# Optimization experiments

Hardware: AMD Instinct MI355X
Metric: run time of the kernel (lower is better)

## Reference

```python
import jax, jax.numpy as jnp
import numpy as np

KERNELS = ("gaussian", "laplacian", "gaussian", "laplacian")
N, M, D, N_PER = 384, 384, 64, 200


def setup_inputs():
    key = jax.random.key(0)
    kx, ky, kb, kp = jax.random.split(key, 4)
    X = jax.random.normal(kx, (N, D), dtype=jnp.float32)
    Y = jax.random.normal(ky, (M, D), dtype=jnp.float32)
    # positive bandwidths of realistic magnitude for d=64 gaussian/laplacian kernels
    bandwidths = jax.random.uniform(kb, (4,), dtype=jnp.float32) * 8.0 + 4.0
    # each row is a random permutation of n+m indices (torch.randperm equivalent)
    perms = jax.vmap(lambda k: jax.random.permutation(k, N + M))(
        jax.random.split(kp, N_PER)).astype(jnp.int32)
    return {"X": X, "Y": Y, "bandwidths": bandwidths, "perms": perms}


def _pairwise_dist(Z):
    # torch.cdist(Z, Z, p=2); eps keeps sqrt grad finite on the zero diagonal
    sq = jnp.sum(Z * Z, axis=1)
    d2 = jnp.maximum(sq[:, None] + sq[None, :] - 2.0 * (Z @ Z.T), 0.0)
    return jnp.sqrt(d2 + 1e-12)


def reference(X, Y, bandwidths, perms):
    n, m = X.shape[0], Y.shape[0]
    Z = jnp.concatenate([X, Y], axis=0)            # [n+m, d]
    dist = _pairwise_dist(Z)                        # [n+m, n+m]
    idx = jnp.arange(min(n, m))
    perm_X, perm_Y = perms[:, :n], perms[:, n:]    # [n_per, n], [n_per, m]
    U, U_b = [], []
    for i, kern in enumerate(KERNELS):
        b = bandwidths[i]
        if kern == "gaussian":
            K = jnp.exp(-(dist * dist) / (b * b))
        else:  # laplacian
            K = jnp.exp(-dist / b)
        # mmd_u's in-place K_XY[diag]=0 mutates the view of K, so zero first
        K = K.at[idx, n + idx].set(0.0)
        K_XX, K_YY, K_XY = K[:n, :n], K[n:, n:], K[:n, n:]
        mmd = ((K_XX.sum() - jnp.trace(K_XX)) / (n * (n - 1))
               + (K_YY.sum() - jnp.trace(K_YY)) / (m * (m - 1))
               - 2.0 * K_XY.sum() / (n * m))
        U.append(mmd)
        # fast_perm: gather permuted blocks, zero diagonals, reduce per permutation
        diagK = jnp.diagonal(K)
        sXX = K[perm_X[:, :, None], perm_X[:, None, :]].sum((1, 2)) - diagK[perm_X].sum(1)
        sYY = K[perm_Y[:, :, None], perm_Y[:, None, :]].sum((1, 2)) - diagK[perm_Y].sum(1)
        sXY = (K[perm_X[:, :, None], perm_Y[:, None, :]].sum((1, 2))
               - K[perm_X[:, idx], perm_Y[:, idx]].sum(1))
        U_b.append(sXX / (n * (n - 1)) + sYY / (m * (m - 1)) - 2.0 * sXY / (n * m))
    U = jnp.stack(U)[:, None]    # [n_b, 1]  == compute_U_stats U.unsqueeze(1)
    U_b = jnp.stack(U_b)         # [n_b, n_per]
    return jnp.concatenate([U, U_b], axis=1)  # [n_b, 1 + n_per]
```

## Files before the change

### kernel.cpp

```cpp
#include <hip/hip_runtime.h>

#define NTOT 768
#define NHALF 384
#define DDIM 64
#define NPER 200
#define PPAD 256
#define NKER 4
#define NMB 12
#define NKH 2
#define NB_GEMM 384
#define NPART (NMB * NKH)
#define NTILE 12
#define LDSROW 68

typedef __attribute__((ext_vector_type(8))) short short8;
typedef __attribute__((ext_vector_type(4))) float floatx4;

constexpr int K0SZ  = NTOT * NTOT;
constexpr int OF_KH = 0;
constexpr int KH_FLOATS = NKER * K0SZ / 2;
constexpr int OF_P   = OF_KH + KH_FLOATS;
constexpr int OF_C   = OF_P + NKER * NTILE * NTOT;
constexpr int OF_ROWM = OF_C + NKER * NHALF;
constexpr int OF_COLM = OF_ROWM + NKER * NTOT;
constexpr int OF_SCAL = OF_COLM + NKER * NTOT;
constexpr int OF_STT  = OF_SCAL + 16;
constexpr int STT_FLOATS = PPAD * NTOT / 2;
constexpr int OF_Q0P  = OF_STT + STT_FLOATS;

__device__ __forceinline__ unsigned short f2bf(float f) {
    unsigned int u = __float_as_uint(f);
    return (unsigned short)((u + 0x7FFFu + ((u >> 16) & 1u)) >> 16);
}
__device__ __forceinline__ float bf2f(unsigned short h) {
    return __uint_as_float(((unsigned int)h) << 16);
}

__global__ __launch_bounds__(256) void k_s1(const float* __restrict__ X,
                                            const float* __restrict__ Y,
                                            const float* __restrict__ bw,
                                            const int* __restrict__ perms,
                                            float* __restrict__ ws) {
    __shared__ float smem[128 * LDSROW + 128];
    float* zb  = smem;
    float* nrm = smem + 128 * LDSROW;
    int bid = blockIdx.x, tid = threadIdx.x;
    unsigned short* STT = (unsigned short*)(ws + OF_STT);
    unsigned short* KH  = (unsigned short*)(ws + OF_KH);

    if (bid < NPER) {
        if (tid < 192) {
            ((uint2*)(STT + bid * NTOT))[tid] = make_uint2(0u, 0u);
            if (bid < PPAD - NPER)
                ((uint2*)(STT + (NPER + bid) * NTOT))[tid] = make_uint2(0u, 0u);
        }
        __syncthreads();
        int v = perms[bid * NTOT + tid];
        STT[bid * NTOT + v] = 0x3F80;
        if (tid < NHALF - 256) {
            int v2 = perms[bid * NTOT + 256 + tid];
            STT[bid * NTOT + v2] = 0x3F80;
        }
        return;
    }

    int t  = bid - NPER;
    int at = t / NTILE, bt = t % NTILE;
    int a0 = at * 64, b0 = bt * 64;
    int ta = tid >> 4, tb = tid & 15;

    float ib2[NKER], ib1[NKER];
#pragma unroll
    for (int k = 0; k < NKER; ++k) { float b = bw[k]; ib2[k] = 1.f / (b * b); ib1[k] = 1.f / b; }

#pragma unroll
    for (int it = 0; it < 8; ++it) {
        int idx = it * 256 + tid;
        int j = idx >> 4, qf = idx & 15;
        int g = (j < 64) ? a0 + j : b0 + (j - 64);
        const float* zr = (g < NHALF) ? X + g * DDIM : Y + (g - NHALF) * DDIM;
        *(float4*)(zb + j * LDSROW + qf * 4) = *(const float4*)(zr + qf * 4);
    }
    __syncthreads();
    if (tid < 128) {
        float s = 0.f;
        const float* zr = zb + tid * LDSROW;
#pragma unroll
        for (int d = 0; d < DDIM; d += 4) {
            float4 zv = *(const float4*)(zr + d);
            s += zv.x * zv.x + zv.y * zv.y + zv.z * zv.z + zv.w * zv.w;
        }
        nrm[tid] = s;
    }
    __syncthreads();

    float acc[4][4];
#pragma unroll
    for (int r = 0; r < 4; ++r)
#pragma unroll
        for (int c = 0; c < 4; ++c) acc[r][c] = 0.f;
#pragma unroll
    for (int s = 0; s < 16; ++s) {
        float4 av[4], bv[4];
#pragma unroll
        for (int r = 0; r < 4; ++r) av[r] = *(const float4*)(zb + (ta * 4 + r) * LDSROW + s * 4);
#pragma unroll
        for (int c = 0; c < 4; ++c) bv[c] = *(const float4*)(zb + (64 + tb * 4 + c) * LDSROW + s * 4);
#pragma unroll
        for (int r = 0; r < 4; ++r)
#pragma unroll
            for (int c = 0; c < 4; ++c) {
                acc[r][c] = fmaf(av[r].x, bv[c].x, acc[r][c]);
                acc[r][c] = fmaf(av[r].y, bv[c].y, acc[r][c]);
                acc[r][c] = fmaf(av[r].z, bv[c].z, acc[r][c]);
                acc[r][c] = fmaf(av[r].w, bv[c].w, acc[r][c]);
            }
    }

    float rs[4][NKER];
#pragma unroll
    for (int r = 0; r < 4; ++r)
#pragma unroll
        for (int k = 0; k < NKER; ++k) rs[r][k] = 0.f;

#pragma unroll
    for (int r = 0; r < 4; ++r) {
        int a = a0 + ta * 4 + r;
        ushort4 us[NKER];
#pragma unroll
        for (int c = 0; c < 4; ++c) {
            int b = b0 + tb * 4 + c;
            float d2 = (nrm[ta * 4 + r] + nrm[64 + tb * 4 + c]) - 2.f * acc[r][c];
            if (b == a) d2 = 0.f;
            d2 = fmaxf(d2, 0.f);
            float d2e = d2 + 1e-12f;
            float dist = sqrtf(d2e);
#pragma unroll
            for (int k = 0; k < NKER; ++k) {
                float val = ((k & 1) == 0) ? __expf(-d2e * ib2[k]) : __expf(-dist * ib1[k]);
                rs[r][k] += val;
                unsigned short h = f2bf(val);
                if (c == 0) us[k].x = h; else if (c == 1) us[k].y = h;
                else if (c == 2) us[k].z = h; else us[k].w = h;
                if (bt == at + 6 && tb == ta && c == r)
                    ws[OF_C + k * NHALF + a] = val;
            }
        }
#pragma unroll
        for (int k = 0; k < NKER; ++k)
            *(ushort4*)(KH + k * K0SZ + a * NTOT + b0 + tb * 4) = us[k];
    }

#pragma unroll
    for (int off = 8; off > 0; off >>= 1)
#pragma unroll
        for (int r = 0; r < 4; ++r)
#pragma unroll
            for (int k = 0; k < NKER; ++k) rs[r][k] += __shfl_down(rs[r][k], off, 64);
    if (tb == 0) {
#pragma unroll
        for (int k = 0; k < NKER; ++k) {
            float4 pv = make_float4(rs[0][k], rs[1][k], rs[2][k], rs[3][k]);
            *(float4*)(ws + OF_P + (k * NTILE + bt) * NTOT + a0 + ta * 4) = pv;
        }
    }
}

__global__ __launch_bounds__(256) void k_s2(const float* __restrict__ bw,
                                            float* __restrict__ ws, float* __restrict__ out) {
    __shared__ float smem[256];
    int bid = blockIdx.x, tid = threadIdx.x;
    int wave = tid >> 6, lane = tid & 63;

    if (bid < NB_GEMM) {
        int mb = bid % NMB;
        int t  = bid / NMB;
        int nc = t & 3;
        int t2 = t >> 2;
        int k  = t2 & 3;
        int kh = t2 >> 2;
        int m0 = mb * 64 + wave * 16;
        int n0 = nc * 64;
        int row = lane & 15, quad = lane >> 4;
        const unsigned short* KH  = (const unsigned short*)(ws + OF_KH);
        const unsigned short* STT = (const unsigned short*)(ws + OF_STT);
        const unsigned short* aptr = KH + k * K0SZ + (m0 + row) * NTOT + quad * 8;
        floatx4 acc[4][2];
#pragma unroll
        for (int j = 0; j < 4; ++j)
#pragma unroll
            for (int h = 0; h < 2; ++h) acc[j][h] = (floatx4){0.f, 0.f, 0.f, 0.f};
        int kk0 = kh * (NTOT / 2);
        for (int kk = kk0; kk < kk0 + NTOT / 2; kk += 64) {
            short8 a0 = *(const short8*)(aptr + kk);
            short8 a1 = *(const short8*)(aptr + kk + 32);
#pragma unroll
            for (int j = 0; j < 4; ++j) {
                const unsigned short* bp = STT + (n0 + j * 16 + row) * NTOT + quad * 8 + kk;
                short8 b0 = *(const short8*)(bp);
                short8 b1 = *(const short8*)(bp + 32);
                acc[j][0] = __builtin_amdgcn_mfma_f32_16x16x32_bf16(a0, b0, acc[j][0], 0, 0, 0);
                acc[j][1] = __builtin_amdgcn_mfma_f32_16x16x32_bf16(a1, b1, acc[j][1], 0, 0, 0);
            }
        }
        __syncthreads();
#pragma unroll
        for (int j = 0; j < 4; ++j) {
            const unsigned short* sp = STT + (n0 + j * 16 + row) * NTOT + m0 + quad * 4;
            float p = 0.f;
#pragma unroll
            for (int r = 0; r < 4; ++r) p += (acc[j][0][r] + acc[j][1][r]) * bf2f(sp[r]);
            p += __shfl_down(p, 32, 64);
            p += __shfl_down(p, 16, 64);
            if (lane < 16) smem[wave * 64 + j * 16 + lane] = p;
        }
        __syncthreads();
        if (tid < 64) {
            float s = smem[tid] + smem[64 + tid] + smem[128 + tid] + smem[192 + tid];
            ws[OF_Q0P + (k * NPART + kh * NMB + mb) * PPAD + n0 + tid] = s;
        }
        return;
    }

    int k = bid - NB_GEMM;
    const float* Pk = ws + OF_P + k * (NTILE * NTOT);
    float v[5] = {0.f, 0.f, 0.f, 0.f, 0.f};
    for (int a = tid; a < NTOT; a += 256) {
        float rsx = 0.f, rsy = 0.f;
#pragma unroll
        for (int j = 0; j < 6; ++j)  rsx += Pk[j * NTOT + a];
#pragma unroll
        for (int j = 6; j < 12; ++j) rsy += Pk[j * NTOT + a];
        float rs0 = rsx + rsy;
        float cx = (a < NHALF)  ? ws[OF_C + k * NHALF + a] : 0.f;
        float cy = (a >= NHALF) ? ws[OF_C + k * NHALF + a - NHALF] : 0.f;
        ws[OF_ROWM + k * NTOT + a] = rs0 - cx;
        ws[OF_COLM + k * NTOT + a] = rs0 - cy;
        v[0] += rs0;
        if (a < NHALF) { v[1] += cx; v[2] += rsx; v[4] += rsy; }
        else           { v[3] += rsy; }
    }
#pragma unroll
    for (int off = 32; off > 0; off >>= 1)
#pragma unroll
        for (int j = 0; j < 5; ++j) v[j] += __shfl_down(v[j], off, 64);
    __syncthreads();
    if (lane == 0)
#pragma unroll
        for (int j = 0; j < 5; ++j) smem[wave * 8 + j] = v[j];
    __syncthreads();
    if (tid == 0) {
        float tot0 = smem[0] + smem[8] + smem[16] + smem[24];
        float csum = smem[1] + smem[9] + smem[17] + smem[25];
        float sxx  = smem[2] + smem[10] + smem[18] + smem[26];
        float syy  = smem[3] + smem[11] + smem[19] + smem[27];
        float sxy  = smem[4] + smem[12] + smem[20] + smem[28];
        float b = bw[k];
        float dist0 = sqrtf(1e-12f);
        float dk = ((k & 1) == 0) ? expf(-(dist0 * dist0) / (b * b)) : expf(-dist0 / b);
        ws[OF_SCAL + k * 4 + 0] = tot0 - csum;
        ws[OF_SCAL + k * 4 + 1] = dk;
        double U = ((double)sxx - 384.0 * (double)dk) * (1.0 / 147072.0)
                 + ((double)syy - 384.0 * (double)dk) * (1.0 / 147072.0)
                 - 2.0 * ((double)sxy - (double)csum) * (1.0 / 147456.0);
        out[k * 201] = (float)U;
    }
}

__global__ __launch_bounds__(256) void k_s3(const int* __restrict__ perms,
                                            const float* __restrict__ ws,
                                            float* __restrict__ out) {
    __shared__ float smem[32];
    int p = blockIdx.x, k = blockIdx.y, tid = threadIdx.x;
    int wave = tid >> 6, lane = tid & 63;
    const unsigned short* STT = (const unsigned short*)(ws + OF_STT);
    const unsigned short* KH  = (const unsigned short*)(ws + OF_KH);
    float v[4] = {0.f, 0.f, 0.f, 0.f};
    for (int i = tid; i < NHALF; i += 256) {
        int a  = perms[p * NTOT + i];
        int bY = perms[p * NTOT + NHALF + i];
        float si  = bf2f(STT[p * NTOT + i]);
        float si2 = bf2f(STT[p * NTOT + NHALF + i]);
        v[0] += ws[OF_ROWM + k * NTOT + a];
        v[1] += ws[OF_COLM + k * NTOT + a];
        float kv = bf2f(KH[k * K0SZ + a * NTOT + bY]);
        if (a < NHALF && bY == a + NHALF) kv = 0.f;
        v[2] += kv;
        v[3] += ws[OF_C + k * NHALF + i] * si * si2;
    }
#pragma unroll
    for (int off = 32; off > 0; off >>= 1)
#pragma unroll
        for (int j = 0; j < 4; ++j) v[j] += __shfl_down(v[j], off, 64);
    if (lane == 0)
#pragma unroll
        for (int j = 0; j < 4; ++j) smem[wave * 4 + j] = v[j];
    __syncthreads();
    if (tid == 0) {
        double rs   = (double)(smem[0] + smem[4] + smem[8]  + smem[12]);
        double cs   = (double)(smem[1] + smem[5] + smem[9]  + smem[13]);
        double pair = (double)(smem[2] + smem[6] + smem[10] + smem[14]);
        double qc   = (double)(smem[3] + smem[7] + smem[11] + smem[15]);
        double total_mod = (double)ws[OF_SCAL + k * 4 + 0];
        double dk        = (double)ws[OF_SCAL + k * 4 + 1];
        double q = -qc;
#pragma unroll
        for (int j = 0; j < NPART; ++j) q += (double)ws[OF_Q0P + (k * NPART + j) * PPAD + p];
        double sXX = q - 384.0 * dk;
        double sYY = total_mod - rs - cs + q - 384.0 * dk;
        double sXY = rs - q - pair;
        out[k * 201 + 1 + p] =
            (float)(sXX * (1.0 / 147072.0) + sYY * (1.0 / 147072.0) - 2.0 * sXY * (1.0 / 147456.0));
    }
}

extern "C" void kernel_launch(void* const* d_in, const int* in_sizes, int n_in,
                              void* d_out, int out_size, void* d_ws, size_t ws_size,
                              hipStream_t stream) {
    const float* X     = (const float*)d_in[0];
    const float* Y     = (const float*)d_in[1];
    const float* bw    = (const float*)d_in[2];
    const int*   perms = (const int*)d_in[3];
    float* ws  = (float*)d_ws;
    float* out = (float*)d_out;

    k_s1<<<NPER + NTILE * NTILE, 256, 0, stream>>>(X, Y, bw, perms, ws);
    k_s2<<<NB_GEMM + NKER, 256, 0, stream>>>(bw, ws, out);
    k_s3<<<dim3(NPER, NKER), 256, 0, stream>>>(perms, ws, out);
}
```

Baseline: 104.7 us.

## Fuse three stages into one cooperative kernel with grid-wide barriers

Merges the three kernels into a single cooperative launch of 400 blocks that uses grid.sync between phases, removing two kernel launch gaps. Phase 3 is restructured so each block handles two kernels per permutation and reduces the partial q values with warp shuffles instead of a serial loop. A fallback to separate launches remains if occupancy or the cooperative launch fails. Grid barriers and the reduced parallelism in phase 3 (400 instead of 800 blocks) are the cost in exchange.

```diff
diff --git a/kernel.cpp b/kernel.cpp
--- a/kernel.cpp
+++ b/kernel.cpp
@@ -1,4 +1,7 @@
 #include <hip/hip_runtime.h>
+#include <hip/hip_cooperative_groups.h>
+
+namespace cg = cooperative_groups;
 
 #define NTOT 768
 #define NHALF 384
@@ -12,6 +15,7 @@
 #define NPART (NMB * NKH)
 #define NTILE 12
 #define LDSROW 68
+#define NBLK_FUSED 400
 
 typedef __attribute__((ext_vector_type(8))) short short8;
 typedef __attribute__((ext_vector_type(4))) float floatx4;
@@ -36,15 +40,14 @@
     return __uint_as_float(((unsigned int)h) << 16);
 }
 
-__global__ __launch_bounds__(256) void k_s1(const float* __restrict__ X,
+__device__ __forceinline__ void phase1_body(int bid, int tid, float* smem,
+                                            const float* __restrict__ X,
                                             const float* __restrict__ Y,
                                             const float* __restrict__ bw,
                                             const int* __restrict__ perms,
                                             float* __restrict__ ws) {
-    __shared__ float smem[128 * LDSROW + 128];
     float* zb  = smem;
     float* nrm = smem + 128 * LDSROW;
-    int bid = blockIdx.x, tid = threadIdx.x;
     unsigned short* STT = (unsigned short*)(ws + OF_STT);
     unsigned short* KH  = (unsigned short*)(ws + OF_KH);
 
@@ -166,10 +169,10 @@
     }
 }
 
-__global__ __launch_bounds__(256) void k_s2(const float* __restrict__ bw,
-                                            float* __restrict__ ws, float* __restrict__ out) {
-    __shared__ float smem[256];
-    int bid = blockIdx.x, tid = threadIdx.x;
+__device__ __forceinline__ void phase2_body(int bid, int tid, float* smem,
+                                            const float* __restrict__ bw,
+                                            float* __restrict__ ws,
+                                            float* __restrict__ out) {
     int wave = tid >> 6, lane = tid & 63;
 
     if (bid < NB_GEMM) {
@@ -267,51 +270,121 @@
     }
 }
 
+__device__ __forceinline__ void phase3_body(int bid, int tid, float* smem,
+                                            const int* __restrict__ perms,
+                                            const float* __restrict__ ws,
+                                            float* __restrict__ out) {
+    int wave = tid >> 6, lane = tid & 63;
+    int p  = bid % NPER;
+    int kb = bid / NPER;
+    int k0 = kb, k1 = kb + 2;
+    const unsigned short* STT = (const unsigned short*)(ws + OF_STT);
+    const unsigned short* KH  = (const unsigned short*)(ws + OF_KH);
+    float v0[4] = {0.f, 0.f, 0.f, 0.f};
+    float v1[4] = {0.f, 0.f, 0.f, 0.f};
+    for (int i = tid; i < NHALF; i += 256) {
+        int a  = perms[p * NTOT + i];
+        int bY = perms[p * NTOT + NHALF + i];
+        float ss = bf2f(STT[p * NTOT + i]) * bf2f(STT[p * NTOT + NHALF + i]);
+        bool diag = (a < NHALF) && (bY == a + NHALF);
+        v0[0] += ws[OF_ROWM + k0 * NTOT + a];
+        v0[1] += ws[OF_COLM + k0 * NTOT + a];
+        float kv0 = bf2f(KH[k0 * K0SZ + a * NTOT + bY]);
+        v0[2] += diag ? 0.f : kv0;
+        v0[3] += ws[OF_C + k0 * NHALF + i] * ss;
+        v1[0] += ws[OF_ROWM + k1 * NTOT + a];
+        v1[1] += ws[OF_COLM + k1 * NTOT + a];
+        float kv1 = bf2f(KH[k1 * K0SZ + a * NTOT + bY]);
+        v1[2] += diag ? 0.f : kv1;
+        v1[3] += ws[OF_C + k1 * NHALF + i] * ss;
+    }
+#pragma unroll
+    for (int off = 32; off > 0; off >>= 1)
+#pragma unroll
+        for (int j = 0; j < 4; ++j) {
+            v0[j] += __shfl_down(v0[j], off, 64);
+            v1[j] += __shfl_down(v1[j], off, 64);
+        }
+    if (lane == 0)
+#pragma unroll
+        for (int j = 0; j < 4; ++j) {
+            smem[wave * 8 + j]     = v0[j];
+            smem[wave * 8 + 4 + j] = v1[j];
+        }
+    float q0 = 0.f, q1 = 0.f;
+    if (tid < NPART) {
+        q0 = ws[OF_Q0P + (k0 * NPART + tid) * PPAD + p];
+        q1 = ws[OF_Q0P + (k1 * NPART + tid) * PPAD + p];
+    }
+#pragma unroll
+    for (int off = 16; off > 0; off >>= 1) {
+        q0 += __shfl_down(q0, off, 32);
+        q1 += __shfl_down(q1, off, 32);
+    }
+    __syncthreads();
+    if (tid == 0) {
+#pragma unroll
+        for (int kk = 0; kk < 2; ++kk) {
+            int k = (kk == 0) ? k0 : k1;
+            int o = (kk == 0) ? 0 : 4;
+            float qsumf = (kk == 0) ? q0 : q1;
+            double rs   = (double)(smem[o + 0] + smem[o + 8] + smem[o + 16] + smem[o + 24]);
+            double cs   = (double)(smem[o + 1] + smem[o + 9] + smem[o + 17] + smem[o + 25]);
+            double pair = (double)(smem[o + 2] + smem[o + 10] + smem[o + 18] + smem[o + 26]);
+            double qc   = (double)(smem[o + 3] + smem[o + 11] + smem[o + 19] + smem[o + 27]);
+            double total_mod = (double)ws[OF_SCAL + k * 4 + 0];
+            double dk        = (double)ws[OF_SCAL + k * 4 + 1];
+            double q = (double)qsumf - qc;
+            double sXX = q - 384.0 * dk;
+            double sYY = total_mod - rs - cs + q - 384.0 * dk;
+            double sXY = rs - q - pair;
+            out[k * 201 + 1 + p] =
+                (float)(sXX * (1.0 / 147072.0) + sYY * (1.0 / 147072.0) - 2.0 * sXY * (1.0 / 147456.0));
+        }
+    }
+}
+
+__global__ __launch_bounds__(256, 2) void k_fused(const float* __restrict__ X,
+                                                  const float* __restrict__ Y,
+                                                  const float* __restrict__ bw,
+                                                  const int* __restrict__ perms,
+                                                  float* __restrict__ ws,
+                                                  float* __restrict__ out) {
+    __shared__ float smem[128 * LDSROW + 128];
+    cg::grid_group grid = cg::this_grid();
+    int bid = blockIdx.x, tid = threadIdx.x;
+
+    if (bid < NPER + NTILE * NTILE) phase1_body(bid, tid, smem, X, Y, bw, perms, ws);
+    __threadfence();
+    grid.sync();
+
+    if (bid < NB_GEMM + NKER) phase2_body(bid, tid, smem, bw, ws, out);
+    __threadfence();
+    grid.sync();
+
+    phase3_body(bid, tid, smem, perms, ws, out);
+}
+
+__global__ __launch_bounds__(256) void k_s1(const float* __restrict__ X,
+                                            const float* __restrict__ Y,
+                                            const float* __restrict__ bw,
+                                            const int* __restrict__ perms,
+                                            float* __restrict__ ws) {
+    __shared__ float smem[128 * LDSROW + 128];
+    phase1_body(blockIdx.x, threadIdx.x, smem, X, Y, bw, perms, ws);
+}
+
+__global__ __launch_bounds__(256) void k_s2(const float* __restrict__ bw,
+                                            float* __restrict__ ws, float* __restrict__ out) {
+    __shared__ float smem[256];
+    phase2_body(blockIdx.x, threadIdx.x, smem, bw, ws, out);
+}
+
 __global__ __launch_bounds__(256) void k_s3(const int* __restrict__ perms,
                                             const float* __restrict__ ws,
                                             float* __restrict__ out) {
-    __shared__ float smem[32];
-    int p = blockIdx.x, k = blockIdx.y, tid = threadIdx.x;
-    int wave = tid >> 6, lane = tid & 63;
-    const unsigned short* STT = (const unsigned short*)(ws + OF_STT);
-    const unsigned short* KH  = (const unsigned short*)(ws + OF_KH);
-    float v[4] = {0.f, 0.f, 0.f, 0.f};
-    for (int i = tid; i < NHALF; i += 256) {
-        int a  = perms[p * NTOT + i];
-        int bY = perms[p * NTOT + NHALF + i];
-        float si  = bf2f(STT[p * NTOT + i]);
-        float si2 = bf2f(STT[p * NTOT + NHALF + i]);
-        v[0] += ws[OF_ROWM + k * NTOT + a];
-        v[1] += ws[OF_COLM + k * NTOT + a];
-        float kv = bf2f(KH[k * K0SZ + a * NTOT + bY]);
-        if (a < NHALF && bY == a + NHALF) kv = 0.f;
-        v[2] += kv;
-        v[3] += ws[OF_C + k * NHALF + i] * si * si2;
-    }
-#pragma unroll
-    for (int off = 32; off > 0; off >>= 1)
-#pragma unroll
-        for (int j = 0; j < 4; ++j) v[j] += __shfl_down(v[j], off, 64);
-    if (lane == 0)
-#pragma unroll
-        for (int j = 0; j < 4; ++j) smem[wave * 4 + j] = v[j];
-    __syncthreads();
-    if (tid == 0) {
-        double rs   = (double)(smem[0] + smem[4] + smem[8]  + smem[12]);
-        double cs   = (double)(smem[1] + smem[5] + smem[9]  + smem[13]);
-        double pair = (double)(smem[2] + smem[6] + smem[10] + smem[14]);
-        double qc   = (double)(smem[3] + smem[7] + smem[11] + smem[15]);
-        double total_mod = (double)ws[OF_SCAL + k * 4 + 0];
-        double dk        = (double)ws[OF_SCAL + k * 4 + 1];
-        double q = -qc;
-#pragma unroll
-        for (int j = 0; j < NPART; ++j) q += (double)ws[OF_Q0P + (k * NPART + j) * PPAD + p];
-        double sXX = q - 384.0 * dk;
-        double sYY = total_mod - rs - cs + q - 384.0 * dk;
-        double sXY = rs - q - pair;
-        out[k * 201 + 1 + p] =
-            (float)(sXX * (1.0 / 147072.0) + sYY * (1.0 / 147072.0) - 2.0 * sXY * (1.0 / 147456.0));
-    }
+    __shared__ float smem[64];
+    phase3_body(blockIdx.x, threadIdx.x, smem, perms, ws, out);
 }
 
 extern "C" void kernel_launch(void* const* d_in, const int* in_sizes, int n_in,
@@ -324,7 +397,20 @@
     float* ws  = (float*)d_ws;
     float* out = (float*)d_out;
 
+    static int coop_ok = -1;
+    if (coop_ok < 0) {
+        int nb = 0;
+        hipError_t e = hipOccupancyMaxActiveBlocksPerMultiprocessor(&nb, k_fused, 256, 0);
+        coop_ok = (e == hipSuccess && nb >= 2) ? 1 : 0;
+    }
+    if (coop_ok == 1) {
+        void* args[6] = {(void*)&X, (void*)&Y, (void*)&bw, (void*)&perms, (void*)&ws, (void*)&out};
+        if (hipLaunchCooperativeKernel(k_fused, dim3(NBLK_FUSED), dim3(256), args, 0u, stream)
+            == hipSuccess)
+            return;
+        coop_ok = 0;
+    }
     k_s1<<<NPER + NTILE * NTILE, 256, 0, stream>>>(X, Y, bw, perms, ws);
     k_s2<<<NB_GEMM + NKER, 256, 0, stream>>>(bw, ws, out);
-    k_s3<<<dim3(NPER, NKER), 256, 0, stream>>>(perms, ws, out);
-}
+    k_s3<<<NBLK_FUSED, 256, 0, stream>>>(perms, ws, out);
+}
```

Result: no change. 102.8 us (-1.8%).
